# Kernel tuning notes

Measured on AMD Instinct MI355X. Metric: run time of the kernel, lower is better.

Reference implementation:

```python
import jax, jax.numpy as jnp
import numpy as np
from jax import lax

B, CIN, COUT, H, W = 2, 256, 128, 128, 128
PPI = 4  # pixels_per_iter


def setup_inputs() -> dict:
    key = jax.random.key(0)
    ks = jax.random.split(key, 10)
    p = lambda k, shp: jax.random.normal(k, shp, jnp.float32) * 0.05
    return {
        "x": jax.random.normal(ks[0], (B, CIN, H, W), jnp.float32),
        "grads": jax.random.normal(ks[1], (B, 2, H, W), jnp.float32),
        "w1": p(ks[2], (COUT, CIN, 1, 1)),          # conv1x1 (bias=False, resnet-style)
        "w2": p(ks[3], (COUT, CIN, 1, 1)),
        "merge_dw": p(ks[4], (2 * COUT, 1, 3, 3)),   # depthwise 3x3
        "merge_pw": p(ks[5], (COUT, 2 * COUT, 1, 1)),# pointwise 1x1
        "merge_b": p(ks[6], (COUT,)),
        "post_dw": p(ks[7], (COUT, 1, 3, 3)),
        "post_pw": p(ks[8], (COUT, COUT, 1, 1)),
        "post_b": p(ks[9], (COUT,)),
    }


def conv2d(x, w, pad=0, groups=1):
    return lax.conv_general_dilated(x, w, (1, 1), [(pad, pad), (pad, pad)],
                                    feature_group_count=groups)


def base_grid(Bn, Hn, Wn):
    # torch affine_grid with identity theta, align_corners=True
    xs = jnp.linspace(-1.0, 1.0, Wn)
    ys = jnp.linspace(-1.0, 1.0, Hn)
    gx, gy = jnp.meshgrid(xs, ys)                      # [H,W] each
    g = jnp.stack([gx, gy], axis=-1)                   # [H,W,2], last dim = (x,y)
    return jnp.broadcast_to(g, (Bn, Hn, Wn, 2))


def grid_sample(img, grid):
    # bilinear, align_corners=True, padding_mode='zeros' (torch defaults)
    Bn, C, Hn, Wn = img.shape
    x = (grid[..., 0] + 1.0) * (Wn - 1) * 0.5          # [B,H,W] pixel coords
    y = (grid[..., 1] + 1.0) * (Hn - 1) * 0.5
    x0 = jnp.floor(x); y0 = jnp.floor(y)
    x1 = x0 + 1.0;     y1 = y0 + 1.0
    wx1 = x - x0; wx0 = 1.0 - wx1
    wy1 = y - y0; wy0 = 1.0 - wy1

    def corner(xi, yi, w):
        valid = (xi >= 0) & (xi <= Wn - 1) & (yi >= 0) & (yi <= Hn - 1)
        xc = jnp.clip(xi, 0, Wn - 1).astype(jnp.int32)
        yc = jnp.clip(yi, 0, Hn - 1).astype(jnp.int32)
        v = jax.vmap(lambda im, yy, xx: im[:, yy, xx])(img, yc, xc)  # [B,C,H,W]
        return v * (w * valid)[:, None]

    return (corner(x0, y0, wx0 * wy0) + corner(x1, y0, wx1 * wy0) +
            corner(x0, y1, wx0 * wy1) + corner(x1, y1, wx1 * wy1))


def reference(x, grads, w1, w2, merge_dw, merge_pw, merge_b, post_dw, post_pw, post_b):
    Bn, _, Hn, Wn = x.shape
    iters = 3 * Hn // (4 * PPI)
    g = (1.5 * grads / iters).transpose(0, 2, 3, 1)    # [B,H,W,2]
    grid = base_grid(Bn, Hn, Wn)
    grid1 = grid + g
    grid2 = grid - g

    m1 = jax.nn.sigmoid(conv2d(x, w1))
    m2 = jax.nn.sigmoid(conv2d(x, w2))

    def step(carry, _):
        a, b, sa, sb = carry
        a = grid_sample(a, grid1)
        b = grid_sample(b, grid2)
        return (a, b, sa + a, sb + b), None

    (_, _, s1, s2), _ = lax.scan(jax.checkpoint(step), (m1, m2, m1, m2), None, length=iters)

    m = jnp.concatenate([jax.nn.sigmoid(s1), jax.nn.sigmoid(s2)], axis=1)  # [B,2*COUT,H,W]
    m = conv2d(conv2d(m, merge_dw, pad=1, groups=2 * COUT), merge_pw) + merge_b[None, :, None, None]
    m = conv2d(conv2d(m, post_dw, pad=1, groups=COUT), post_pw) + post_b[None, :, None, None]
    return m
```

## Files before the change

### kernel.cpp

```cpp
#include <hip/hip_runtime.h>
#include <hip/hip_fp16.h>


#define PC 4194304
#define HW 16384

struct CoefC { int4 o0; float4 w0; int4 o1; float4 w1; int4 o2; float4 w2; int4 o3; float4 w3; };
struct Coef1 { int4 oa; float4 wa; };

struct alignas(16) H8 { __half2 h[4]; };
struct alignas(8)  H4 { __half2 h[2]; };
typedef _Float16 f16x8 __attribute__((ext_vector_type(8)));
typedef float f32x4 __attribute__((ext_vector_type(4)));

__device__ __forceinline__ float sigf(float v) { return 1.0f / (1.0f + __expf(-v)); }

__device__ __forceinline__ H8 f8h(const float* f) {
  H8 r;
#pragma unroll
  for (int i = 0; i < 4; i++) r.h[i] = __floats2half2_rn(f[2*i], f[2*i+1]);
  return r;
}
__device__ __forceinline__ f16x8 ld8(const __half* p) { return *(const f16x8*)p; }
__device__ __forceinline__ void fma8(float* a, const f16x8& v, float w) {
#pragma unroll
  for (int i = 0; i < 8; i++) a[i] = fmaf(w, (float)v[i], a[i]);
}

template <int SPB>
__device__ __forceinline__ int slot_base_64k(int bid) {
  int xcd = bid & 7;
  int i = xcd >> 1;
  int half = xcd & 1;
  int sub = bid >> 3;
  return (i >> 1) * 32768 + (i & 1) * 16384 + half * 8192 + sub * SPB;
}
template <int SPB>
__device__ __forceinline__ int slot_base_32k(int bid) {
  int xcd = bid & 7;
  int b = xcd >> 2;
  int q = xcd & 3;
  int sub = bid >> 3;
  return b * 16384 + q * 4096 + sub * SPB;
}

__device__ __forceinline__ void stencil(const float* __restrict__ g, float sgn, int pix,
                                        int4& op, float4& wt) {
  int b = pix >> 14, hw = pix & 16383;
  int h = hw >> 7, w = hw & 127;
  float gx = g[(size_t)(b * 2 + 0) * HW + hw];
  float gy = g[(size_t)(b * 2 + 1) * HW + hw];
  float xp = (float)w + sgn * gx;
  float yp = (float)h + sgn * gy;
  float x0f = floorf(xp), y0f = floorf(yp);
  float fx = xp - x0f, fy = yp - y0f;
  int x0 = (int)x0f, y0 = (int)y0f;
  int x1 = x0 + 1, y1 = y0 + 1;
  bool vx0 = (x0 >= 0) && (x0 <= 127);
  bool vx1 = (x1 >= 0) && (x1 <= 127);
  bool vy0 = (y0 >= 0) && (y0 <= 127);
  bool vy1 = (y1 >= 0) && (y1 <= 127);
  int x0c = min(max(x0, 0), 127), x1c = min(max(x1, 0), 127);
  int y0c = min(max(y0, 0), 127), y1c = min(max(y1, 0), 127);
  int bb = b << 14;
  op.x = bb + y0c * 128 + x0c;
  op.y = bb + y0c * 128 + x1c;
  op.z = bb + y1c * 128 + x0c;
  op.w = bb + y1c * 128 + x1c;
  wt.x = (vx0 && vy0) ? (1.f - fx) * (1.f - fy) : 0.f;
  wt.y = (vx1 && vy0) ? fx * (1.f - fy) : 0.f;
  wt.z = (vx0 && vy1) ? (1.f - fx) * fy : 0.f;
  wt.w = (vx1 && vy1) ? fx * fy : 0.f;
}

__device__ __forceinline__ int4 shl7(int4 v) {
  return make_int4(v.x << 7, v.y << 7, v.z << 7, v.w << 7);
}
__device__ __forceinline__ float4 scale4(float4 v, float s) {
  return make_float4(v.x * s, v.y * s, v.z * s, v.w * s);
}

__global__ __launch_bounds__(256) void prep_kernel(const float* __restrict__ grads,
                                                   Coef1* __restrict__ c1,
                                                   CoefC* __restrict__ c2,
                                                   const float* __restrict__ mdw,
                                                   const float* __restrict__ pdw,
                                                   const float* __restrict__ w1,
                                                   const float* __restrict__ w2,
                                                   const float* __restrict__ mpw,
                                                   const float* __restrict__ ppw,
                                                   float* __restrict__ wdwT,
                                                   float* __restrict__ pdwT,
                                                   __half* __restrict__ wT16,
                                                   __half* __restrict__ wpw1,
                                                   __half* __restrict__ wpw2) {
  int bid = blockIdx.x;
  int tid = threadIdx.x;
  if (bid < 256) {
    int idx = bid * 256 + tid;
    int chain = idx >> 15;
    int p = idx & 32767;
    float sgn = chain ? -3.96875f : 3.96875f;
    int4 op; float4 ow;
    stencil(grads, sgn, p, op, ow);
    Coef1 a; a.oa = shl7(op); a.wa = ow;
    c1[idx] = a;
    CoefC c;
    int4 o2; float4 nw;
    stencil(grads, sgn, op.x, o2, nw); c.o0 = shl7(o2); c.w0 = scale4(nw, ow.x);
    stencil(grads, sgn, op.y, o2, nw); c.o1 = shl7(o2); c.w1 = scale4(nw, ow.y);
    stencil(grads, sgn, op.z, o2, nw); c.o2 = shl7(o2); c.w2 = scale4(nw, ow.z);
    stencil(grads, sgn, op.w, o2, nw); c.o3 = shl7(o2); c.w3 = scale4(nw, ow.w);
    c2[idx] = c;
  } else {
    int i = (bid - 256) * 256 + tid;
    if (i < 65536) {
      int co = i >> 8, ci = i & 255;
      float v = (co < 128) ? w1[co * 256 + ci] : w2[(size_t)(co - 128) * 256 + ci];
      wT16[i] = __float2half(v);
    } else if (i < 98304) {
      int j = i - 65536;
      wpw1[j] = __float2half(mpw[j]);
    } else if (i < 114688) {
      int j = i - 98304;
      wpw2[j] = __float2half(ppw[j]);
    } else if (i < 116992) {
      int j = i - 114688;
      int ch = j / 9, t = j % 9;
      wdwT[t * 256 + ch] = mdw[j];
    } else if (i < 118144) {
      int j = i - 116992;
      int ch = j / 9, t = j % 9;
      pdwT[t * 128 + ch] = pdw[j];
    }
  }
}

__global__ __launch_bounds__(256) void conv1_kernel(const float* __restrict__ x,
                                                    const __half* __restrict__ wT16,
                                                    __half* __restrict__ mOut) {
  __shared__ __align__(16) char As[4096];
  __shared__ __align__(16) char Bs[16384];
  int tid = threadIdx.x;
  int p0 = blockIdx.x * 64;
  int b = p0 >> 14;
  int hw0 = p0 & 16383;
  int wv = tid >> 6, ln = tid & 63;
  int hi = ln >> 4, lo = ln & 15;
  f32x4 acc[4][4] = {};
  const float* xb = x + (size_t)b * 256 * HW + hw0;
  int apx = tid & 63, ac8 = (tid >> 6) * 8;
  int abyte = (apx * 64 + ac8 * 2) ^ ((apx & 3) << 4);
  for (int k = 0; k < 256; k += 32) {
    f16x8 av;
#pragma unroll
    for (int j = 0; j < 8; j++) av[j] = (_Float16)xb[(size_t)(k + ac8 + j) * HW + apx];
    if (k) __syncthreads();
    *(f16x8*)(As + abyte) = av;
    {
      const __half* src = wT16 + (size_t)tid * 256 + k;
#pragma unroll
      for (int s = 0; s < 4; s++) {
        f16x8 bv = *(const f16x8*)(src + s * 8);
        int byte = (tid * 64 + s * 16) ^ ((tid & 3) << 4);
        *(f16x8*)(Bs + byte) = bv;
      }
    }
    __syncthreads();
    f16x8 aF[4], bF[4];
#pragma unroll
    for (int m = 0; m < 4; m++) {
      int px = m * 16 + lo;
      int byte = (px * 64 + hi * 16) ^ ((px & 3) << 4);
      aF[m] = *(const f16x8*)(As + byte);
    }
#pragma unroll
    for (int n = 0; n < 4; n++) {
      int co = wv * 64 + n * 16 + lo;
      int byte = (co * 64 + hi * 16) ^ ((co & 3) << 4);
      bF[n] = *(const f16x8*)(Bs + byte);
    }
#pragma unroll
    for (int m = 0; m < 4; m++)
#pragma unroll
      for (int n = 0; n < 4; n++)
        acc[m][n] = __builtin_amdgcn_mfma_f32_16x16x32_f16(aF[m], bF[n], acc[m][n], 0, 0, 0);
  }
  size_t base = (wv >= 2) ? (size_t)PC : 0;
  int col0 = (wv & 1) * 64;
#pragma unroll
  for (int m = 0; m < 4; m++)
#pragma unroll
    for (int n = 0; n < 4; n++) {
      int col = col0 + n * 16 + lo;
#pragma unroll
      for (int rr = 0; rr < 4; rr++) {
        int px = p0 + m * 16 + hi * 4 + rr;
        mOut[base + (size_t)px * 128 + col] = __float2half(sigf(acc[m][n][rr]));
      }
    }
}

template <int ACC>
__global__ __launch_bounds__(256) void s2_kernel(const __half* __restrict__ inb,
                                                 __half* __restrict__ outb,
                                                 const __half* __restrict__ accAdd,
                                                 __half* __restrict__ accOut,
                                                 const uint4* __restrict__ c2tab) {
  __shared__ uint4 cs[128];
  int tid = threadIdx.x;
  int slot0 = slot_base_64k<16>(blockIdx.x);
  if (tid < 128) cs[tid] = c2tab[(size_t)slot0 * 8 + tid];
  __syncthreads();
  const CoefC c = ((const CoefC*)cs)[tid >> 4];
  int slot = slot0 + (tid >> 4);
  int ch = (tid & 15) << 3;
  int chain = slot >> 15;
  size_t cb = (size_t)chain * PC;
  const __half* base = inb + cb + ch;
  int rowel = ((slot & 32767) << 7) + ch;

  float a2[8] = {};
  f16x8 p0 = ld8(base + c.o0.x), p1 = ld8(base + c.o0.y),
        p2 = ld8(base + c.o0.z), p3 = ld8(base + c.o0.w);
  f16x8 q0 = ld8(base + c.o1.x), q1 = ld8(base + c.o1.y),
        q2 = ld8(base + c.o1.z), q3 = ld8(base + c.o1.w);
  fma8(a2, p0, c.w0.x); fma8(a2, p1, c.w0.y); fma8(a2, p2, c.w0.z); fma8(a2, p3, c.w0.w);
  p0 = ld8(base + c.o2.x); p1 = ld8(base + c.o2.y);
  p2 = ld8(base + c.o2.z); p3 = ld8(base + c.o2.w);
  fma8(a2, q0, c.w1.x); fma8(a2, q1, c.w1.y); fma8(a2, q2, c.w1.z); fma8(a2, q3, c.w1.w);
  q0 = ld8(base + c.o3.x); q1 = ld8(base + c.o3.y);
  q2 = ld8(base + c.o3.z); q3 = ld8(base + c.o3.w);
  fma8(a2, p0, c.w2.x); fma8(a2, p1, c.w2.y); fma8(a2, p2, c.w2.z); fma8(a2, p3, c.w2.w);
  fma8(a2, q0, c.w3.x); fma8(a2, q1, c.w3.y); fma8(a2, q2, c.w3.z); fma8(a2, q3, c.w3.w);

  *(H8*)(outb + cb + rowel) = f8h(a2);
  if (ACC == 1) {
    f16x8 av = ld8(accAdd + cb + rowel);
    float af[8];
#pragma unroll
    for (int i = 0; i < 8; i++) af[i] = a2[i] + (float)av[i];
    *(H8*)(accOut + cb + rowel) = f8h(af);
  } else if (ACC == 2) {
    f16x8 av = ld8(accOut + cb + rowel);
    float af[8];
#pragma unroll
    for (int i = 0; i < 8; i++) af[i] = a2[i] + (float)av[i];
    *(H8*)(accOut + cb + rowel) = f8h(af);
  }
}

__global__ __launch_bounds__(256) void fin_kernel(const __half* __restrict__ tb,
                                                  const __half* __restrict__ mb,
                                                  const uint4* __restrict__ c1tab,
                                                  const uint4* __restrict__ c2tab,
                                                  __half* __restrict__ outb) {
  __shared__ uint4 c2s[128];
  __shared__ uint4 c1s[32];
  int tid = threadIdx.x;
  int slot0 = slot_base_64k<16>(blockIdx.x);
  if (tid < 128) c2s[tid] = c2tab[(size_t)slot0 * 8 + tid];
  if (tid < 32)  c1s[tid] = c1tab[(size_t)slot0 * 2 + tid];
  __syncthreads();
  const CoefC c = ((const CoefC*)c2s)[tid >> 4];
  const Coef1 a = ((const Coef1*)c1s)[tid >> 4];
  int slot = slot0 + (tid >> 4);
  int ch = (tid & 15) << 3;
  int chain = slot >> 15;
  size_t cb = (size_t)chain * PC;
  const __half* base = tb + cb + ch;
  int rowel = ((slot & 32767) << 7) + ch;

  float r[8] = {};
  f16x8 p0 = ld8(base + a.oa.x), p1 = ld8(base + a.oa.y),
        p2 = ld8(base + a.oa.z), p3 = ld8(base + a.oa.w);
  f16x8 q0 = ld8(base + c.o0.x), q1 = ld8(base + c.o0.y),
        q2 = ld8(base + c.o0.z), q3 = ld8(base + c.o0.w);
  fma8(r, p0, a.wa.x); fma8(r, p1, a.wa.y); fma8(r, p2, a.wa.z); fma8(r, p3, a.wa.w);
  p0 = ld8(base + c.o1.x); p1 = ld8(base + c.o1.y);
  p2 = ld8(base + c.o1.z); p3 = ld8(base + c.o1.w);
  fma8(r, q0, c.w0.x); fma8(r, q1, c.w0.y); fma8(r, q2, c.w0.z); fma8(r, q3, c.w0.w);
  q0 = ld8(base + c.o2.x); q1 = ld8(base + c.o2.y);
  q2 = ld8(base + c.o2.z); q3 = ld8(base + c.o2.w);
  fma8(r, p0, c.w1.x); fma8(r, p1, c.w1.y); fma8(r, p2, c.w1.z); fma8(r, p3, c.w1.w);
  p0 = ld8(base + c.o3.x); p1 = ld8(base + c.o3.y);
  p2 = ld8(base + c.o3.z); p3 = ld8(base + c.o3.w);
  fma8(r, q0, c.w2.x); fma8(r, q1, c.w2.y); fma8(r, q2, c.w2.z); fma8(r, q3, c.w2.w);
  fma8(r, p0, c.w3.x); fma8(r, p1, c.w3.y); fma8(r, p2, c.w3.z); fma8(r, p3, c.w3.w);

  f16x8 mv = ld8(mb + cb + rowel);
#pragma unroll
  for (int i = 0; i < 8; i++) r[i] = sigf(r[i] + (float)mv[i]);
  *(H8*)(outb + cb + rowel) = f8h(r);
}

template <int C>
__global__ __launch_bounds__(256) void dw_kernel(const __half* __restrict__ in,
                                                 const float* __restrict__ wT,
                                                 __half* __restrict__ out) {
  int tid = threadIdx.x;
  constexpr int TPP = C / 8;
  constexpr int PPB = 256 / TPP;
  int slot = slot_base_32k<PPB>(blockIdx.x) + tid / TPP;
  int ch = (tid % TPP) * 8;
  int b = slot >> 14, h = (slot >> 7) & 127, w = slot & 127;
  const __half* src;
  int choff;
  if (C == 256) { src = in + ((ch < 128) ? 0 : (size_t)PC); choff = ch & 127; }
  else          { src = in; choff = ch; }
  float acc[8] = {};
#pragma unroll
  for (int t = 0; t < 9; t++) {
    int dy = t / 3 - 1, dx = t % 3 - 1;
    int yy = h + dy, xx = w + dx;
    if (yy < 0 || yy > 127 || xx < 0 || xx > 127) continue;
    int q = (b << 14) + yy * 128 + xx;
    f16x8 v = ld8(src + (size_t)q * 128 + choff);
    float4 wa = *(const float4*)(wT + t * C + ch);
    float4 wb = *(const float4*)(wT + t * C + ch + 4);
    acc[0] = fmaf(wa.x, (float)v[0], acc[0]);
    acc[1] = fmaf(wa.y, (float)v[1], acc[1]);
    acc[2] = fmaf(wa.z, (float)v[2], acc[2]);
    acc[3] = fmaf(wa.w, (float)v[3], acc[3]);
    acc[4] = fmaf(wb.x, (float)v[4], acc[4]);
    acc[5] = fmaf(wb.y, (float)v[5], acc[5]);
    acc[6] = fmaf(wb.z, (float)v[6], acc[6]);
    acc[7] = fmaf(wb.w, (float)v[7], acc[7]);
  }
  *(H8*)(out + (size_t)slot * C + ch) = f8h(acc);
}

__global__ __launch_bounds__(256) void pw1_kernel(const __half* __restrict__ in,
                                                  const __half* __restrict__ w16,
                                                  const float* __restrict__ bias,
                                                  __half* __restrict__ out) {
  int tid = threadIdx.x;
  int p0 = blockIdx.x * 64;
  int wv = tid >> 6, ln = tid & 63;
  int hi = ln >> 4, lo = ln & 15;
  int px = p0 + wv * 16 + lo;
  f32x4 acc[8] = {};
  for (int k = 0; k < 256; k += 32) {
    f16x8 bF = *(const f16x8*)(in + (size_t)px * 256 + k + hi * 8);
#pragma unroll
    for (int m = 0; m < 8; m++) {
      f16x8 aF = *(const f16x8*)(w16 + (size_t)(m * 16 + lo) * 256 + k + hi * 8);
      acc[m] = __builtin_amdgcn_mfma_f32_16x16x32_f16(aF, bF, acc[m], 0, 0, 0);
    }
  }
  int opx = p0 + wv * 16 + lo;
#pragma unroll
  for (int m = 0; m < 8; m++) {
    int co = m * 16 + hi * 4;
    float4 bv = *(const float4*)(bias + co);
    H4 hv;
    hv.h[0] = __floats2half2_rn(acc[m][0] + bv.x, acc[m][1] + bv.y);
    hv.h[1] = __floats2half2_rn(acc[m][2] + bv.z, acc[m][3] + bv.w);
    *(H4*)(out + (size_t)opx * 128 + co) = hv;
  }
}

__global__ __launch_bounds__(256) void pw2_kernel(const __half* __restrict__ in,
                                                  const __half* __restrict__ w16,
                                                  const float* __restrict__ bias,
                                                  float* __restrict__ out) {
  int tid = threadIdx.x;
  int p0 = blockIdx.x * 64;
  int b = p0 >> 14;
  int hw0 = p0 & 16383;
  int wv = tid >> 6, ln = tid & 63;
  int hi = ln >> 4, lo = ln & 15;
  int co0 = wv * 32;
  f32x4 acc[4][2] = {};
  for (int k = 0; k < 128; k += 32) {
    f16x8 aF[4], bF[2];
#pragma unroll
    for (int m = 0; m < 4; m++)
      aF[m] = *(const f16x8*)(in + (size_t)(p0 + m * 16 + lo) * 128 + k + hi * 8);
#pragma unroll
    for (int n = 0; n < 2; n++)
      bF[n] = *(const f16x8*)(w16 + (size_t)(co0 + n * 16 + lo) * 128 + k + hi * 8);
#pragma unroll
    for (int m = 0; m < 4; m++)
#pragma unroll
      for (int n = 0; n < 2; n++)
        acc[m][n] = __builtin_amdgcn_mfma_f32_16x16x32_f16(aF[m], bF[n], acc[m][n], 0, 0, 0);
  }
#pragma unroll
  for (int m = 0; m < 4; m++)
#pragma unroll
    for (int n = 0; n < 2; n++) {
      int co = co0 + n * 16 + lo;
      float bb = bias[co];
      float4 v = {acc[m][n][0] + bb, acc[m][n][1] + bb, acc[m][n][2] + bb, acc[m][n][3] + bb};
      *(float4*)(out + (size_t)(b * 128 + co) * HW + hw0 + m * 16 + hi * 4) = v;
    }
}

extern "C" void kernel_launch(void* const* d_in, const int* in_sizes, int n_in,
                              void* d_out, int out_size, void* d_ws, size_t ws_size,
                              hipStream_t stream) {
  const float* x     = (const float*)d_in[0];
  const float* grads = (const float*)d_in[1];
  const float* w1    = (const float*)d_in[2];
  const float* w2    = (const float*)d_in[3];
  const float* mdw   = (const float*)d_in[4];
  const float* mpw   = (const float*)d_in[5];
  const float* mb    = (const float*)d_in[6];
  const float* pdw   = (const float*)d_in[7];
  const float* ppw   = (const float*)d_in[8];
  const float* pb    = (const float*)d_in[9];
  float* out = (float*)d_out;
  char* wsb = (char*)d_ws;

  __half* M  = (__half*)wsb;
  __half* A  = (__half*)(wsb + (size_t)16777216);
  __half* Bb = (__half*)(wsb + (size_t)33554432);
  __half* Pb = (__half*)(wsb + (size_t)50331648);
  __half* Qb = (__half*)(wsb + (size_t)67108864);
  CoefC* C2  = (CoefC*)(wsb + (size_t)83886080);
  Coef1* C1  = (Coef1*)(wsb + (size_t)92274688);
  __half* WT16 = (__half*)(wsb + (size_t)94371840);
  __half* WPW1 = (__half*)(wsb + (size_t)94502912);
  __half* WPW2 = (__half*)(wsb + (size_t)94568448);
  float* wdwT  = (float*)(wsb + (size_t)94601216);
  float* pdwT  = wdwT + 2304;

  const uint4* c2u = (const uint4*)C2;
  const uint4* c1u = (const uint4*)C1;

  prep_kernel<<<718, 256, 0, stream>>>(grads, C1, C2, mdw, pdw, w1, w2, mpw, ppw,
                                       wdwT, pdwT, WT16, WPW1, WPW2);
  conv1_kernel<<<512, 256, 0, stream>>>(x, WT16, M);

  s2_kernel<0><<<4096, 256, 0, stream>>>(M,  A,  nullptr, nullptr, c2u);
  s2_kernel<0><<<4096, 256, 0, stream>>>(A,  Bb, nullptr, nullptr, c2u);
  s2_kernel<0><<<4096, 256, 0, stream>>>(Bb, A,  nullptr, nullptr, c2u);
  s2_kernel<1><<<4096, 256, 0, stream>>>(A,  Bb, M,       Pb,      c2u);
  s2_kernel<0><<<4096, 256, 0, stream>>>(Bb, A,  nullptr, nullptr, c2u);
  s2_kernel<0><<<4096, 256, 0, stream>>>(A,  Bb, nullptr, nullptr, c2u);
  s2_kernel<0><<<4096, 256, 0, stream>>>(Bb, A,  nullptr, nullptr, c2u);
  s2_kernel<2><<<4096, 256, 0, stream>>>(A,  Bb, nullptr, Pb,      c2u);
  s2_kernel<0><<<4096, 256, 0, stream>>>(Pb, A,  nullptr, nullptr, c2u);
  s2_kernel<1><<<4096, 256, 0, stream>>>(A,  Bb, Pb,      Qb,      c2u);
  s2_kernel<1><<<4096, 256, 0, stream>>>(Qb, A,  Qb,      Pb,      c2u);
  fin_kernel<<<4096, 256, 0, stream>>>(Pb, M, c1u, c2u, A);

  __half* DW1 = Bb;
  __half* PW1 = Qb;
  __half* DW2 = Qb + PC;
  dw_kernel<256><<<4096, 256, 0, stream>>>(A, wdwT, DW1);
  pw1_kernel<<<512, 256, 0, stream>>>(DW1, WPW1, mb, PW1);
  dw_kernel<128><<<2048, 256, 0, stream>>>(PW1, pdwT, DW2);
  pw2_kernel<<<512, 256, 0, stream>>>(DW2, WPW2, pb, out);
}
```

Before: 268.2 us.

## Use 2D pixel tiles per block and split final stencil into two single-step passes

Blocks now map their 16 pixels to a 4x4 spatial tile instead of 16 consecutive pixels in a row, aiming to improve cache locality of the bilinear gather neighbors. The fused final kernel, which applied a single-step stencil plus a composed four-tap-set stencil, is replaced by two single-step kernels (accumulate then sigmoid). This trades one heavier gather kernel with 20 loads per thread for two lighter ones with an extra intermediate write/read.

```diff
diff --git a/kernel.cpp b/kernel.cpp
--- a/kernel.cpp
+++ b/kernel.cpp
@@ -26,14 +26,21 @@
 #pragma unroll
   for (int i = 0; i < 8; i++) a[i] = fmaf(w, (float)v[i], a[i]);
 }
-
-template <int SPB>
-__device__ __forceinline__ int slot_base_64k(int bid) {
+__device__ __forceinline__ void fma4g(float* a, const f16x8& v0, const f16x8& v1,
+                                      const f16x8& v2, const f16x8& v3, float4 w) {
+  fma8(a, v0, w.x); fma8(a, v1, w.y); fma8(a, v2, w.z); fma8(a, v3, w.w);
+}
+
+__device__ __forceinline__ int slot_of_64k(int bid, int sgi) {
   int xcd = bid & 7;
-  int i = xcd >> 1;
+  int img = xcd >> 1;
   int half = xcd & 1;
   int sub = bid >> 3;
-  return (i >> 1) * 32768 + (i & 1) * 16384 + half * 8192 + sub * SPB;
+  int tc = sub & 31;
+  int tr = sub >> 5;
+  int r = half * 64 + tr * 4 + (sgi >> 2);
+  int c = tc * 4 + (sgi & 3);
+  return (img >> 1) * 32768 + (img & 1) * 16384 + r * 128 + c;
 }
 template <int SPB>
 __device__ __forceinline__ int slot_base_32k(int bid) {
@@ -209,11 +216,14 @@
                                                  const uint4* __restrict__ c2tab) {
   __shared__ uint4 cs[128];
   int tid = threadIdx.x;
-  int slot0 = slot_base_64k<16>(blockIdx.x);
-  if (tid < 128) cs[tid] = c2tab[(size_t)slot0 * 8 + tid];
+  if (tid < 128) {
+    int sgi = tid >> 3, word = tid & 7;
+    int sl = slot_of_64k(blockIdx.x, sgi);
+    cs[tid] = c2tab[(size_t)sl * 8 + word];
+  }
   __syncthreads();
   const CoefC c = ((const CoefC*)cs)[tid >> 4];
-  int slot = slot0 + (tid >> 4);
+  int slot = slot_of_64k(blockIdx.x, tid >> 4);
   int ch = (tid & 15) << 3;
   int chain = slot >> 15;
   size_t cb = (size_t)chain * PC;
@@ -225,14 +235,14 @@
         p2 = ld8(base + c.o0.z), p3 = ld8(base + c.o0.w);
   f16x8 q0 = ld8(base + c.o1.x), q1 = ld8(base + c.o1.y),
         q2 = ld8(base + c.o1.z), q3 = ld8(base + c.o1.w);
-  fma8(a2, p0, c.w0.x); fma8(a2, p1, c.w0.y); fma8(a2, p2, c.w0.z); fma8(a2, p3, c.w0.w);
+  fma4g(a2, p0, p1, p2, p3, c.w0);
   p0 = ld8(base + c.o2.x); p1 = ld8(base + c.o2.y);
   p2 = ld8(base + c.o2.z); p3 = ld8(base + c.o2.w);
-  fma8(a2, q0, c.w1.x); fma8(a2, q1, c.w1.y); fma8(a2, q2, c.w1.z); fma8(a2, q3, c.w1.w);
+  fma4g(a2, q0, q1, q2, q3, c.w1);
   q0 = ld8(base + c.o3.x); q1 = ld8(base + c.o3.y);
   q2 = ld8(base + c.o3.z); q3 = ld8(base + c.o3.w);
-  fma8(a2, p0, c.w2.x); fma8(a2, p1, c.w2.y); fma8(a2, p2, c.w2.z); fma8(a2, p3, c.w2.w);
-  fma8(a2, q0, c.w3.x); fma8(a2, q1, c.w3.y); fma8(a2, q2, c.w3.z); fma8(a2, q3, c.w3.w);
+  fma4g(a2, p0, p1, p2, p3, c.w2);
+  fma4g(a2, q0, q1, q2, q3, c.w3);
 
   *(H8*)(outb + cb + rowel) = f8h(a2);
   if (ACC == 1) {
@@ -250,47 +260,38 @@
   }
 }
 
-__global__ __launch_bounds__(256) void fin_kernel(const __half* __restrict__ tb,
-                                                  const __half* __restrict__ mb,
-                                                  const uint4* __restrict__ c1tab,
-                                                  const uint4* __restrict__ c2tab,
-                                                  __half* __restrict__ outb) {
-  __shared__ uint4 c2s[128];
-  __shared__ uint4 c1s[32];
-  int tid = threadIdx.x;
-  int slot0 = slot_base_64k<16>(blockIdx.x);
-  if (tid < 128) c2s[tid] = c2tab[(size_t)slot0 * 8 + tid];
-  if (tid < 32)  c1s[tid] = c1tab[(size_t)slot0 * 2 + tid];
+template <int MODE>
+__global__ __launch_bounds__(256) void s1_kernel(const __half* __restrict__ tin,
+                                                 const __half* __restrict__ own,
+                                                 __half* __restrict__ outb,
+                                                 const uint4* __restrict__ c1tab) {
+  __shared__ uint4 cs[32];
+  int tid = threadIdx.x;
+  if (tid < 32) {
+    int sgi = tid >> 1, word = tid & 1;
+    int sl = slot_of_64k(blockIdx.x, sgi);
+    cs[tid] = c1tab[(size_t)sl * 2 + word];
+  }
   __syncthreads();
-  const CoefC c = ((const CoefC*)c2s)[tid >> 4];
-  const Coef1 a = ((const Coef1*)c1s)[tid >> 4];
-  int slot = slot0 + (tid >> 4);
+  const Coef1 a = ((const Coef1*)cs)[tid >> 4];
+  int slot = slot_of_64k(blockIdx.x, tid >> 4);
   int ch = (tid & 15) << 3;
   int chain = slot >> 15;
   size_t cb = (size_t)chain * PC;
-  const __half* base = tb + cb + ch;
+  const __half* base = tin + cb + ch;
   int rowel = ((slot & 32767) << 7) + ch;
-
+  f16x8 t0 = ld8(base + a.oa.x), t1 = ld8(base + a.oa.y),
+        t2 = ld8(base + a.oa.z), t3 = ld8(base + a.oa.w);
+  f16x8 ov = ld8(own + cb + rowel);
   float r[8] = {};
-  f16x8 p0 = ld8(base + a.oa.x), p1 = ld8(base + a.oa.y),
-        p2 = ld8(base + a.oa.z), p3 = ld8(base + a.oa.w);
-  f16x8 q0 = ld8(base + c.o0.x), q1 = ld8(base + c.o0.y),
-        q2 = ld8(base + c.o0.z), q3 = ld8(base + c.o0.w);
-  fma8(r, p0, a.wa.x); fma8(r, p1, a.wa.y); fma8(r, p2, a.wa.z); fma8(r, p3, a.wa.w);
-  p0 = ld8(base + c.o1.x); p1 = ld8(base + c.o1.y);
-  p2 = ld8(base + c.o1.z); p3 = ld8(base + c.o1.w);
-  fma8(r, q0, c.w0.x); fma8(r, q1, c.w0.y); fma8(r, q2, c.w0.z); fma8(r, q3, c.w0.w);
-  q0 = ld8(base + c.o2.x); q1 = ld8(base + c.o2.y);
-  q2 = ld8(base + c.o2.z); q3 = ld8(base + c.o2.w);
-  fma8(r, p0, c.w1.x); fma8(r, p1, c.w1.y); fma8(r, p2, c.w1.z); fma8(r, p3, c.w1.w);
-  p0 = ld8(base + c.o3.x); p1 = ld8(base + c.o3.y);
-  p2 = ld8(base + c.o3.z); p3 = ld8(base + c.o3.w);
-  fma8(r, q0, c.w2.x); fma8(r, q1, c.w2.y); fma8(r, q2, c.w2.z); fma8(r, q3, c.w2.w);
-  fma8(r, p0, c.w3.x); fma8(r, p1, c.w3.y); fma8(r, p2, c.w3.z); fma8(r, p3, c.w3.w);
-
-  f16x8 mv = ld8(mb + cb + rowel);
-#pragma unroll
-  for (int i = 0; i < 8; i++) r[i] = sigf(r[i] + (float)mv[i]);
+  fma4g(r, t0, t1, t2, t3, a.wa);
+  if (MODE == 0) {
+#pragma unroll
+    for (int i = 0; i < 8; i++) r[i] += (float)ov[i];
+  } else {
+#pragma unroll
+    for (int i = 0; i < 8; i++) r[i] = sigf(r[i] + (float)ov[i]);
+  }
   *(H8*)(outb + cb + rowel) = f8h(r);
 }
 
@@ -444,7 +445,8 @@
   s2_kernel<0><<<4096, 256, 0, stream>>>(Pb, A,  nullptr, nullptr, c2u);
   s2_kernel<1><<<4096, 256, 0, stream>>>(A,  Bb, Pb,      Qb,      c2u);
   s2_kernel<1><<<4096, 256, 0, stream>>>(Qb, A,  Qb,      Pb,      c2u);
-  fin_kernel<<<4096, 256, 0, stream>>>(Pb, M, c1u, c2u, A);
+  s1_kernel<0><<<4096, 256, 0, stream>>>(Pb, Pb, Bb, c1u);
+  s1_kernel<1><<<4096, 256, 0, stream>>>(Bb, M,  A,  c1u);
 
   __half* DW1 = Bb;
   __half* PW1 = Qb;
```

After: 273.8 us. +2.1%, slower.
